# Kernel optimization log

Hardware: AMD Instinct MI355X
Metric: run time of the kernel (lower is better)

## Reference

```python
import jax, jax.numpy as jnp
from jax import lax
import numpy as np

N_LABELS = 48
START = 46
END = 47


def _viterbi_forward(emission_scores, transition, lengths):
    # scores[b, t, i, j]: score of transitioning from label i to label j at step t
    scores = emission_scores + transition  # [B, T, L, L]
    B, T, L, _ = scores.shape
    lengths = lengths.astype(jnp.int32)

    # ---- t == 0 ----
    mask0 = (lengths > 0)[:, None]  # [B, 1]
    first = scores[:, 0, START, :]  # [B, L]
    best0 = jnp.where(mask0, first, 0.0)
    upto0 = jnp.where(mask0, first, 0.0)
    bp0 = jnp.where(mask0, jnp.int32(START), jnp.int32(END))
    bp0 = jnp.broadcast_to(bp0, (B, L))

    # ---- t = 1 .. T-1 via scan (inherently sequential DP) ----
    def step(carry, inp):
        best, upto = carry  # each [B, L]
        s_t, t = inp  # s_t: [B, L, L]
        mask = (lengths > t)[:, None]  # [B, 1]
        cand = s_t + best[:, :, None]  # [B, from, to]
        new_best = jnp.max(cand, axis=1)  # [B, L]
        bp = jnp.argmax(cand, axis=1).astype(jnp.int32)  # [B, L]
        new_upto = jax.scipy.special.logsumexp(s_t + upto[:, :, None], axis=1)
        best = jnp.where(mask, new_best, best)
        upto = jnp.where(mask, new_upto, upto)
        bp = jnp.where(mask, bp, jnp.int32(END))
        return (best, upto), bp

    ts = jnp.arange(1, T, dtype=jnp.int32)
    scores_rest = jnp.swapaxes(scores[:, 1:], 0, 1)  # [T-1, B, L, L]
    (best, upto), bps = lax.scan(step, (best0, upto0), (scores_rest, ts))
    backpointers = jnp.concatenate([bp0[None], bps], axis=0)  # [T, B, L]

    # ---- backtracking (reverse scan over time) ----
    pointer0 = jnp.full((B,), END, dtype=jnp.int32)

    def back(ptr, bp_t):  # bp_t: [B, L]
        dec = jnp.take_along_axis(bp_t, ptr[:, None], axis=1)[:, 0]
        return dec, dec

    _, decoded = lax.scan(back, pointer0, backpointers, reverse=True)  # [T, B]
    decoded = decoded.T  # [B, T]
    # drop the initial start-label column, append end label
    decoded = jnp.concatenate(
        [decoded[:, 1:], jnp.full((B, 1), END, dtype=decoded.dtype)], axis=1
    )
    score_out = -(upto[:, END] - best[:, END])  # [B]
    return decoded, score_out


def setup_inputs() -> dict:
    key = jax.random.key(0)
    k1, k2, k3 = jax.random.split(key, 3)
    B, T, L = 32, 256, N_LABELS
    emission_scores = jax.random.normal(k1, (B, T, L, L), dtype=jnp.float32)
    transition = jax.random.normal(k2, (L, L), dtype=jnp.float32)
    lengths = jax.random.randint(k3, (B,), 128, T + 1, dtype=jnp.int64)
    lengths = lengths.at[0].set(T)  # ensure max(lengths) == T (padded length)
    return {"emission_scores": emission_scores, "transition": transition, "lengths": lengths}


def reference(emission_scores, transition, lengths):
    return _viterbi_forward(emission_scores, transition, lengths)
```

## Files before the change

### kernel.cpp

```cpp
#include <hip/hip_runtime.h>


#define TT 256
#define LL 48
#define LSTART 46
#define LEND 47
#define BB 32
#define NL 64

#define BARRIER() do { \
    asm volatile("s_waitcnt lgkmcnt(0)" ::: "memory"); \
    __builtin_amdgcn_s_barrier(); \
  } while (0)

#define LOADROW(BUF, ROW) do { \
    int r_ = (ROW) < (TT - 1) ? (ROW) : (TT - 1); \
    const float* q_ = base + (size_t)r_ * (LL*LL); \
    _Pragma("unroll") \
    for (int k = 0; k < 12; ++k) (BUF)[k] = q_[k*LL]; \
  } while (0)

#define AMAX(vx, ix, vy, iy) do { \
    if ((vy) > (vx)) { (vx) = (vy); (ix) = (iy); } } while (0)

#define RL(var, lane) __int_as_float(__builtin_amdgcn_readlane(__float_as_int(var), (lane)))

#define STEP_V(BUF, T_, PAR) do { \
    float cv[12]; int ci[12]; \
    _Pragma("unroll") \
    for (int k = 0; k < 12; ++k) { \
      cv[k] = (BUF)[k] + trg[k] + RL(vbest, 12*w + k); \
      ci[k] = 12*w + k; \
    } \
    AMAX(cv[0],ci[0],cv[1],ci[1]);  AMAX(cv[2],ci[2],cv[3],ci[3]); \
    AMAX(cv[4],ci[4],cv[5],ci[5]);  AMAX(cv[6],ci[6],cv[7],ci[7]); \
    AMAX(cv[8],ci[8],cv[9],ci[9]);  AMAX(cv[10],ci[10],cv[11],ci[11]); \
    AMAX(cv[0],ci[0],cv[2],ci[2]);  AMAX(cv[4],ci[4],cv[6],ci[6]); \
    AMAX(cv[8],ci[8],cv[10],ci[10]); \
    AMAX(cv[0],ci[0],cv[4],ci[4]); \
    AMAX(cv[0],ci[0],cv[8],ci[8]); \
    partV[PAR][w][j] = make_float2(cv[0], __int_as_float(ci[0])); \
    BARRIER(); \
    float2 m0 = partV[PAR][0][j], m1 = partV[PAR][1][j]; \
    float2 m2 = partV[PAR][2][j], m3 = partV[PAR][3][j]; \
    float bv = m0.x; int ba = __float_as_int(m0.y); \
    AMAX(bv, ba, m1.x, __float_as_int(m1.y)); \
    AMAX(bv, ba, m2.x, __float_as_int(m2.y)); \
    AMAX(bv, ba, m3.x, __float_as_int(m3.y)); \
    bool upd = act && ((T_) < len); \
    vbest = upd ? bv : vbest; \
    if (w == 0 && upd) bp[(T_)*LL + j] = (unsigned char)ba; \
  } while (0)

#define STEP_L(BUF, T_, PAR) do { \
    float e[12]; \
    _Pragma("unroll") \
    for (int k = 0; k < 12; ++k) { \
      float x = (BUF)[k] + trg[k] + RL(vupto, 12*w + k); \
      e[k] = exp2f((x - msh) * 1.44269504f); \
    } \
    float s01 = e[0]+e[1], s23 = e[2]+e[3], s45 = e[4]+e[5]; \
    float s67 = e[6]+e[7], s89 = e[8]+e[9], sab = e[10]+e[11]; \
    float ps = ((s01+s23)+(s45+s67)) + (s89+sab); \
    partS[PAR][w][j] = ps; \
    BARRIER(); \
    float sum = partS[PAR][0][j] + partS[PAR][1][j] \
              + partS[PAR][2][j] + partS[PAR][3][j]; \
    float nu = msh + log2f(sum) * 0.69314718056f; \
    bool upd = act && ((T_) < len); \
    vupto = upd ? nu : vupto; \
    msh = RL(vupto, 0); \
  } while (0)

__launch_bounds__(256, 1)
__global__ void viterbi_fwd(const float* __restrict__ em,
                            const float* __restrict__ tr,
                            const int* __restrict__ len_raw,
                            float* __restrict__ out,
                            float* __restrict__ ws)
{
  const int role = blockIdx.x >> 5;
  const int b    = blockIdx.x & 31;
  const int tid  = threadIdx.x;
  const int w    = tid >> 6;
  const int j    = tid & 63;
  const bool act = (j < LL);
  const int jl   = act ? j : (LL - 1);

  int len;
  {
    bool is64 = (len_raw[1] == 0) && (len_raw[3] == 0) && (len_raw[5] == 0);
    len = is64 ? len_raw[2*b] : len_raw[b];
    if (len > TT) len = TT;
    if (len < 1) len = 1;
  }

  __shared__ float2 partV[2][4][NL];
  __shared__ float  partS[2][4][NL];
  __shared__ unsigned char bp[TT*LL];
  __shared__ unsigned char cmp_[16*LL];
  __shared__ unsigned char entry_[16];
  __shared__ unsigned char raw[TT];

  float trg[12];
  #pragma unroll
  for (int k = 0; k < 12; ++k) trg[k] = tr[(12*w + k)*LL + jl];

  const float init = em[(size_t)b*TT*LL*LL + LSTART*LL + jl] + tr[LSTART*LL + jl];

  const float* base = em + (size_t)b*TT*LL*LL + (size_t)(12*w)*LL + jl;
  float b0[12], b1[12], b2[12], b3[12];

  if (role == 0) {
    for (int idx = tid; idx < LL; idx += 256) bp[idx] = (unsigned char)LSTART;
    for (int idx = len*LL + tid; idx < TT*LL; idx += 256) bp[idx] = (unsigned char)LEND;

    float vbest = act ? init : -INFINITY;
    LOADROW(b0, 1); LOADROW(b1, 2); LOADROW(b2, 3);
    int t = 1;
    #pragma unroll 1
    for (int it = 0; it < 63; ++it) {
      LOADROW(b3, t + 3); STEP_V(b0, t,     0);
      LOADROW(b0, t + 4); STEP_V(b1, t + 1, 1);
      LOADROW(b1, t + 5); STEP_V(b2, t + 2, 0);
      LOADROW(b2, t + 6); STEP_V(b3, t + 3, 1);
      t += 4;
    }
    STEP_V(b0, 253, 0); STEP_V(b1, 254, 1); STEP_V(b2, 255, 0);

    if (tid == LEND) ws[BB + b] = vbest;
    __syncthreads();

    for (int idx = tid; idx < 16*LL; idx += 256) {
      int c = idx / LL, l = idx - c*LL;
      int pc = l;
      #pragma unroll
      for (int k = 15; k >= 0; --k) pc = bp[(16*c + k)*LL + pc];
      cmp_[c*LL + l] = (unsigned char)pc;
    }
    __syncthreads();
    if (tid == 0) {
      int pc = LEND;
      for (int c = 15; c >= 0; --c) { entry_[c] = (unsigned char)pc; pc = cmp_[c*LL + pc]; }
    }
    __syncthreads();
    if (tid < 16) {
      int c = tid, pc = entry_[c];
      #pragma unroll
      for (int k = 15; k >= 0; --k) { int t2 = 16*c + k; pc = bp[t2*LL + pc]; raw[t2] = (unsigned char)pc; }
    }
    __syncthreads();
    out[(size_t)b*TT + tid] = (tid < TT - 1) ? (float)raw[tid + 1] : (float)LEND;
  } else {
    float vupto = act ? init : -INFINITY;
    float msh = RL(vupto, 0);
    LOADROW(b0, 1); LOADROW(b1, 2); LOADROW(b2, 3);
    int t = 1;
    #pragma unroll 1
    for (int it = 0; it < 63; ++it) {
      LOADROW(b3, t + 3); STEP_L(b0, t,     0);
      LOADROW(b0, t + 4); STEP_L(b1, t + 1, 1);
      LOADROW(b1, t + 5); STEP_L(b2, t + 2, 0);
      LOADROW(b2, t + 6); STEP_L(b3, t + 3, 1);
      t += 4;
    }
    STEP_L(b0, 253, 0); STEP_L(b1, 254, 1); STEP_L(b2, 255, 0);

    if (tid == LEND) ws[b] = vupto;
  }
}

__global__ void viterbi_score(const float* __restrict__ ws, float* __restrict__ out)
{
  int b = threadIdx.x;
  if (b < BB) out[(size_t)BB*TT + b] = ws[BB + b] - ws[b];
}

extern "C" void kernel_launch(void* const* d_in, const int* in_sizes, int n_in,
                              void* d_out, int out_size, void* d_ws, size_t ws_size,
                              hipStream_t stream) {
  const float* em  = (const float*)d_in[0];
  const float* tr  = (const float*)d_in[1];
  const int*   ln  = (const int*)d_in[2];
  float* out = (float*)d_out;
  float* ws  = (float*)d_ws;
  viterbi_fwd<<<dim3(64), dim3(256), 0, stream>>>(em, tr, ln, out, ws);
  viterbi_score<<<dim3(1), dim3(64), 0, stream>>>(ws, out);
}
```

Measured before the change: 144.3 us.

## Stream emission rows into an LDS ring via async global_load_lds prefetch

Replaces per-thread register prefetch of emission rows with asynchronous global-to-LDS loads into an 8-row shared ring buffer, issued in groups of four rows and waited on once per four steps. Each step reads the next row from LDS and precomputes emission+transition (scaled to log2 domain for the logsumexp path) ahead of the barrier. The Viterbi path also splits value and index partials, and only wave 0 resolves the argmax. The goal is to hide global memory latency behind the sequential DP, at the cost of much larger LDS usage and fragile hand-managed vmcnt waits.

```diff
diff --git a/kernel.cpp b/kernel.cpp
--- a/kernel.cpp
+++ b/kernel.cpp
@@ -1,37 +1,46 @@
 #include <hip/hip_runtime.h>
+#include <stdint.h>
 
 
 #define TT 256
 #define LL 48
+#define ROWF 2304
 #define LSTART 46
 #define LEND 47
 #define BB 32
 #define NL 64
-
-#define BARRIER() do { \
-    asm volatile("s_waitcnt lgkmcnt(0)" ::: "memory"); \
-    __builtin_amdgcn_s_barrier(); \
+#define LOG2E 1.44269504088896f
+#define LN2 0.693147180559945f
+
+#define GLL(GP, LP) __builtin_amdgcn_global_load_lds( \
+    (const __attribute__((address_space(1))) void*)(GP), \
+    (__attribute__((address_space(3))) void*)(LP), 16, 0, 0)
+
+#define FENCE() asm volatile("" ::: "memory")
+#define WAIT_PLAIN() asm volatile("s_waitcnt lgkmcnt(0)" ::: "memory")
+#define WAIT_VM0()   asm volatile("s_waitcnt vmcnt(0) lgkmcnt(0)" ::: "memory")
+
+#define AMAX(vx, ix, vy, iy) do { if ((vy) > (vx)) { (vx)=(vy); (ix)=(iy);} } while(0)
+#define RL(var, lane) __int_as_float(__builtin_amdgcn_readlane(__float_as_int(var), (lane)))
+
+#define ISSUE_GROUP(GR0, HB) do { \
+    const float* gs_ = em_lane + (size_t)(GR0)*ROWF; \
+    float* ls_ = ring + (HB); \
+    _Pragma("unroll") \
+    for (int ii = 0; ii < 9; ++ii) \
+      GLL(gs_ + (w*9+ii)*256, ls_ + (w*9+ii)*256); \
   } while (0)
 
-#define LOADROW(BUF, ROW) do { \
-    int r_ = (ROW) < (TT - 1) ? (ROW) : (TT - 1); \
-    const float* q_ = base + (size_t)r_ * (LL*LL); \
-    _Pragma("unroll") \
-    for (int k = 0; k < 12; ++k) (BUF)[k] = q_[k*LL]; \
-  } while (0)
-
-#define AMAX(vx, ix, vy, iy) do { \
-    if ((vy) > (vx)) { (vx) = (vy); (ix) = (iy); } } while (0)
-
-#define RL(var, lane) __int_as_float(__builtin_amdgcn_readlane(__float_as_int(var), (lane)))
-
-#define STEP_V(BUF, T_, PAR) do { \
+#define STEP_V(ETRC, ETRN, T_, WAITM) do { \
+    const int PAR_ = (T_) & 1; \
+    float en_[12]; \
+    { const float* lp_ = ring + (size_t)(((T_)+1)&7)*ROWF + jl; \
+      _Pragma("unroll") \
+      for (int k = 0; k < 12; ++k) en_[k] = lp_[(12*w+k)*LL]; } \
     float cv[12]; int ci[12]; \
     _Pragma("unroll") \
     for (int k = 0; k < 12; ++k) { \
-      cv[k] = (BUF)[k] + trg[k] + RL(vbest, 12*w + k); \
-      ci[k] = 12*w + k; \
-    } \
+      cv[k] = (ETRC)[k] + RL(vbest, lanebase+k); ci[k] = lanebase+k; } \
     AMAX(cv[0],ci[0],cv[1],ci[1]);  AMAX(cv[2],ci[2],cv[3],ci[3]); \
     AMAX(cv[4],ci[4],cv[5],ci[5]);  AMAX(cv[6],ci[6],cv[7],ci[7]); \
     AMAX(cv[8],ci[8],cv[9],ci[9]);  AMAX(cv[10],ci[10],cv[11],ci[11]); \
@@ -39,37 +48,53 @@
     AMAX(cv[8],ci[8],cv[10],ci[10]); \
     AMAX(cv[0],ci[0],cv[4],ci[4]); \
     AMAX(cv[0],ci[0],cv[8],ci[8]); \
-    partV[PAR][w][j] = make_float2(cv[0], __int_as_float(ci[0])); \
-    BARRIER(); \
-    float2 m0 = partV[PAR][0][j], m1 = partV[PAR][1][j]; \
-    float2 m2 = partV[PAR][2][j], m3 = partV[PAR][3][j]; \
-    float bv = m0.x; int ba = __float_as_int(m0.y); \
-    AMAX(bv, ba, m1.x, __float_as_int(m1.y)); \
-    AMAX(bv, ba, m2.x, __float_as_int(m2.y)); \
-    AMAX(bv, ba, m3.x, __float_as_int(m3.y)); \
-    bool upd = act && ((T_) < len); \
-    vbest = upd ? bv : vbest; \
-    if (w == 0 && upd) bp[(T_)*LL + j] = (unsigned char)ba; \
+    partVal[PAR_][w][j] = cv[0]; \
+    partIdx[PAR_][w][j] = ci[0]; \
+    _Pragma("unroll") \
+    for (int k = 0; k < 12; ++k) (ETRN)[k] = en_[k] + trg[k]; \
+    WAITM(); \
+    __builtin_amdgcn_s_barrier(); \
+    FENCE(); \
+    float v0_ = partVal[PAR_][0][j], v1_ = partVal[PAR_][1][j]; \
+    float v2_ = partVal[PAR_][2][j], v3_ = partVal[PAR_][3][j]; \
+    const bool upd_ = act && ((T_) < len); \
+    float bv_ = fmaxf(fmaxf(v0_, v1_), fmaxf(v2_, v3_)); \
+    vbest = upd_ ? bv_ : vbest; \
+    if (w == 0 && upd_) { \
+      float bx_ = v0_; int ba_ = partIdx[PAR_][0][j]; \
+      AMAX(bx_, ba_, v1_, partIdx[PAR_][1][j]); \
+      AMAX(bx_, ba_, v2_, partIdx[PAR_][2][j]); \
+      AMAX(bx_, ba_, v3_, partIdx[PAR_][3][j]); \
+      bp[(T_)*LL + j] = (unsigned char)ba_; \
+    } \
   } while (0)
 
-#define STEP_L(BUF, T_, PAR) do { \
-    float e[12]; \
+#define STEP_L(ETRC, ETRN, T_, WAITM) do { \
+    const int PAR_ = (T_) & 1; \
+    float en_[12]; \
+    { const float* lp_ = ring + (size_t)(((T_)+1)&7)*ROWF + jl; \
+      _Pragma("unroll") \
+      for (int k = 0; k < 12; ++k) en_[k] = lp_[(12*w+k)*LL]; } \
+    float ex[12]; \
     _Pragma("unroll") \
     for (int k = 0; k < 12; ++k) { \
-      float x = (BUF)[k] + trg[k] + RL(vupto, 12*w + k); \
-      e[k] = exp2f((x - msh) * 1.44269504f); \
+      float d_ = (ETRC)[k] - msh2; \
+      ex[k] = exp2f(d_ + RL(vupto2, lanebase+k)); \
     } \
-    float s01 = e[0]+e[1], s23 = e[2]+e[3], s45 = e[4]+e[5]; \
-    float s67 = e[6]+e[7], s89 = e[8]+e[9], sab = e[10]+e[11]; \
-    float ps = ((s01+s23)+(s45+s67)) + (s89+sab); \
-    partS[PAR][w][j] = ps; \
-    BARRIER(); \
-    float sum = partS[PAR][0][j] + partS[PAR][1][j] \
-              + partS[PAR][2][j] + partS[PAR][3][j]; \
-    float nu = msh + log2f(sum) * 0.69314718056f; \
-    bool upd = act && ((T_) < len); \
-    vupto = upd ? nu : vupto; \
-    msh = RL(vupto, 0); \
+    float s01=ex[0]+ex[1], s23=ex[2]+ex[3], s45=ex[4]+ex[5]; \
+    float s67=ex[6]+ex[7], s89=ex[8]+ex[9], sab=ex[10]+ex[11]; \
+    partVal[PAR_][w][j] = ((s01+s23)+(s45+s67))+(s89+sab); \
+    _Pragma("unroll") \
+    for (int k = 0; k < 12; ++k) (ETRN)[k] = (en_[k] + trg[k]) * LOG2E; \
+    WAITM(); \
+    __builtin_amdgcn_s_barrier(); \
+    FENCE(); \
+    float sum_ = (partVal[PAR_][0][j] + partVal[PAR_][1][j]) \
+               + (partVal[PAR_][2][j] + partVal[PAR_][3][j]); \
+    float nu_ = msh2 + __log2f(sum_); \
+    const bool upd_ = act && ((T_) < len); \
+    vupto2 = upd_ ? nu_ : vupto2; \
+    msh2 = RL(vupto2, 0); \
   } while (0)
 
 __launch_bounds__(256, 1)
@@ -86,6 +111,7 @@
   const int j    = tid & 63;
   const bool act = (j < LL);
   const int jl   = act ? j : (LL - 1);
+  const int lanebase = 12*w;
 
   int len;
   {
@@ -95,38 +121,51 @@
     if (len < 1) len = 1;
   }
 
-  __shared__ float2 partV[2][4][NL];
-  __shared__ float  partS[2][4][NL];
+  __shared__ float ring[8*ROWF];
+  __shared__ float partVal[2][4][NL];
+  __shared__ int   partIdx[2][4][NL];
   __shared__ unsigned char bp[TT*LL];
   __shared__ unsigned char cmp_[16*LL];
   __shared__ unsigned char entry_[16];
   __shared__ unsigned char raw[TT];
 
+  const float* em_lane = em + (size_t)b*TT*ROWF + 4*j;
+
   float trg[12];
   #pragma unroll
-  for (int k = 0; k < 12; ++k) trg[k] = tr[(12*w + k)*LL + jl];
-
-  const float init = em[(size_t)b*TT*LL*LL + LSTART*LL + jl] + tr[LSTART*LL + jl];
-
-  const float* base = em + (size_t)b*TT*LL*LL + (size_t)(12*w)*LL + jl;
-  float b0[12], b1[12], b2[12], b3[12];
+  for (int k = 0; k < 12; ++k) trg[k] = tr[(12*w+k)*LL + jl];
+
+  ISSUE_GROUP(0, 0);
+  ISSUE_GROUP(4, 4*ROWF);
+  asm volatile("s_waitcnt vmcnt(9)" ::: "memory");
+  __builtin_amdgcn_s_barrier();
+  FENCE();
+
+  const float init = ring[LSTART*LL + jl] + tr[LSTART*LL + jl];
 
   if (role == 0) {
     for (int idx = tid; idx < LL; idx += 256) bp[idx] = (unsigned char)LSTART;
     for (int idx = len*LL + tid; idx < TT*LL; idx += 256) bp[idx] = (unsigned char)LEND;
 
     float vbest = act ? init : -INFINITY;
-    LOADROW(b0, 1); LOADROW(b1, 2); LOADROW(b2, 3);
-    int t = 1;
+    float etrA[12], etrB[12];
+    { const float* lp_ = ring + ROWF + jl;
+      #pragma unroll
+      for (int k = 0; k < 12; ++k) etrA[k] = lp_[(12*w+k)*LL] + trg[k]; }
+
     #pragma unroll 1
     for (int it = 0; it < 63; ++it) {
-      LOADROW(b3, t + 3); STEP_V(b0, t,     0);
-      LOADROW(b0, t + 4); STEP_V(b1, t + 1, 1);
-      LOADROW(b1, t + 5); STEP_V(b2, t + 2, 0);
-      LOADROW(b2, t + 6); STEP_V(b3, t + 3, 1);
-      t += 4;
-    }
-    STEP_V(b0, 253, 0); STEP_V(b1, 254, 1); STEP_V(b2, 255, 0);
+      const int t0 = 4*it + 1;
+      STEP_V(etrA, etrB, t0,     WAIT_PLAIN);
+      STEP_V(etrB, etrA, t0 + 1, WAIT_VM0);
+      { int gr0 = 4*it + 8; if (gr0 > 252) gr0 = 252;
+        ISSUE_GROUP(gr0, (size_t)(it & 1)*4*ROWF); }
+      STEP_V(etrA, etrB, t0 + 2, WAIT_PLAIN);
+      STEP_V(etrB, etrA, t0 + 3, WAIT_PLAIN);
+    }
+    STEP_V(etrA, etrB, 253, WAIT_PLAIN);
+    STEP_V(etrB, etrA, 254, WAIT_VM0);
+    STEP_V(etrA, etrB, 255, WAIT_PLAIN);
 
     if (tid == LEND) ws[BB + b] = vbest;
     __syncthreads();
@@ -152,21 +191,28 @@
     __syncthreads();
     out[(size_t)b*TT + tid] = (tid < TT - 1) ? (float)raw[tid + 1] : (float)LEND;
   } else {
-    float vupto = act ? init : -INFINITY;
-    float msh = RL(vupto, 0);
-    LOADROW(b0, 1); LOADROW(b1, 2); LOADROW(b2, 3);
-    int t = 1;
+    float vupto2 = act ? init * LOG2E : -INFINITY;
+    float msh2 = RL(vupto2, 0);
+    float etrA[12], etrB[12];
+    { const float* lp_ = ring + ROWF + jl;
+      #pragma unroll
+      for (int k = 0; k < 12; ++k) etrA[k] = (lp_[(12*w+k)*LL] + trg[k]) * LOG2E; }
+
     #pragma unroll 1
     for (int it = 0; it < 63; ++it) {
-      LOADROW(b3, t + 3); STEP_L(b0, t,     0);
-      LOADROW(b0, t + 4); STEP_L(b1, t + 1, 1);
-      LOADROW(b1, t + 5); STEP_L(b2, t + 2, 0);
-      LOADROW(b2, t + 6); STEP_L(b3, t + 3, 1);
-      t += 4;
-    }
-    STEP_L(b0, 253, 0); STEP_L(b1, 254, 1); STEP_L(b2, 255, 0);
-
-    if (tid == LEND) ws[b] = vupto;
+      const int t0 = 4*it + 1;
+      STEP_L(etrA, etrB, t0,     WAIT_PLAIN);
+      STEP_L(etrB, etrA, t0 + 1, WAIT_VM0);
+      { int gr0 = 4*it + 8; if (gr0 > 252) gr0 = 252;
+        ISSUE_GROUP(gr0, (size_t)(it & 1)*4*ROWF); }
+      STEP_L(etrA, etrB, t0 + 2, WAIT_PLAIN);
+      STEP_L(etrB, etrA, t0 + 3, WAIT_PLAIN);
+    }
+    STEP_L(etrA, etrB, 253, WAIT_PLAIN);
+    STEP_L(etrB, etrA, 254, WAIT_VM0);
+    STEP_L(etrA, etrB, 255, WAIT_PLAIN);
+
+    if (tid == LEND) ws[b] = vupto2 * LN2;
   }
 }
 
```

Result: slower. 155.5 us (+7.8%).

## Stage emission rows via global_load_lds ring and switch logsumexp to linear-domain scaling

Applied to the files above, without the earlier changes.

Emission rows are now prefetched asynchronously into a six-slot LDS ring with global_load_lds, replacing per-thread register prefetch. The loop is software-pipelined so the reduction of the previous step overlaps with computing the next step's partials, with one barrier per step. The logsumexp path now works in the probability domain: it exponentiates emissions plus transitions independently of the recurrence, combines them with FMAs against a scaled state vector, and renormalises by extracting the exponent, which removes the per-step log and the dependence of exp on the carried state. The risks are precision and underflow in the scaled linear domain, plus the extra LDS footprint and the subtle ring-slot and vmcnt bookkeeping.

```diff
diff --git a/kernel.cpp b/kernel.cpp
--- a/kernel.cpp
+++ b/kernel.cpp
@@ -3,35 +3,43 @@
 
 #define TT 256
 #define LL 48
+#define ROWF 2304
 #define LSTART 46
 #define LEND 47
 #define BB 32
-#define NL 64
+#define LOG2E 1.44269504088896f
+#define LN2 0.693147180559945f
+
+#define GLL16(GP, LP) __builtin_amdgcn_global_load_lds( \
+    (const __attribute__((address_space(1))) void*)(GP), \
+    (__attribute__((address_space(3))) void*)(LP), 16, 0, 0)
+#define GLL4(GP, LP) __builtin_amdgcn_global_load_lds( \
+    (const __attribute__((address_space(1))) void*)(GP), \
+    (__attribute__((address_space(3))) void*)(LP), 4, 0, 0)
+
+#define RL(var, lane) __int_as_float(__builtin_amdgcn_readlane(__float_as_int(var), (lane)))
 
 #define BARRIER() do { \
     asm volatile("s_waitcnt lgkmcnt(0)" ::: "memory"); \
     __builtin_amdgcn_s_barrier(); \
   } while (0)
-
-#define LOADROW(BUF, ROW) do { \
-    int r_ = (ROW) < (TT - 1) ? (ROW) : (TT - 1); \
-    const float* q_ = base + (size_t)r_ * (LL*LL); \
-    _Pragma("unroll") \
-    for (int k = 0; k < 12; ++k) (BUF)[k] = q_[k*LL]; \
-  } while (0)
-
-#define AMAX(vx, ix, vy, iy) do { \
-    if ((vy) > (vx)) { (vx) = (vy); (ix) = (iy); } } while (0)
-
-#define RL(var, lane) __int_as_float(__builtin_amdgcn_readlane(__float_as_int(var), (lane)))
-
-#define STEP_V(BUF, T_, PAR) do { \
+#define WAITVM(N) asm volatile("s_waitcnt vmcnt(" #N ")" ::: "memory")
+
+#define AMAX(vx, ix, vy, iy) do { if ((vy) > (vx)) { (vx)=(vy); (ix)=(iy);} } while(0)
+
+#define STAGE(ROW, SLOT) do { \
+    const float* gs_ = emB + (size_t)(ROW)*ROWF + wslice; \
+    float* ls_ = ring + (SLOT)*ROWF + wslice; \
+    GLL16(gs_ + 4*j, ls_); \
+    GLL16(gs_ + 256 + 4*j, ls_ + 256); \
+    GLL4 (gs_ + 512 + j, ls_ + 512); \
+  } while (0)
+
+#define PARTIALS_V(ETR, PW) do { \
     float cv[12]; int ci[12]; \
     _Pragma("unroll") \
     for (int k = 0; k < 12; ++k) { \
-      cv[k] = (BUF)[k] + trg[k] + RL(vbest, 12*w + k); \
-      ci[k] = 12*w + k; \
-    } \
+      cv[k] = (ETR)[k] + RL(vbest, 12*w + k); ci[k] = 12*w + k; } \
     AMAX(cv[0],ci[0],cv[1],ci[1]);  AMAX(cv[2],ci[2],cv[3],ci[3]); \
     AMAX(cv[4],ci[4],cv[5],ci[5]);  AMAX(cv[6],ci[6],cv[7],ci[7]); \
     AMAX(cv[8],ci[8],cv[9],ci[9]);  AMAX(cv[10],ci[10],cv[11],ci[11]); \
@@ -39,38 +47,78 @@
     AMAX(cv[8],ci[8],cv[10],ci[10]); \
     AMAX(cv[0],ci[0],cv[4],ci[4]); \
     AMAX(cv[0],ci[0],cv[8],ci[8]); \
-    partV[PAR][w][j] = make_float2(cv[0], __int_as_float(ci[0])); \
+    partV[PW][w][j] = make_float2(cv[0], __int_as_float(ci[0])); \
+  } while (0)
+
+#define ITER_V(T_, RAWP, RAWN) do { \
+    const int pr_ = ((T_)-1) & 1; \
+    float2 m0_ = partV[pr_][0][j], m1_ = partV[pr_][1][j]; \
+    float2 m2_ = partV[pr_][2][j], m3_ = partV[pr_][3][j]; \
+    float etr_[12]; \
+    _Pragma("unroll") \
+    for (int k = 0; k < 12; ++k) etr_[k] = (RAWP)[k] + trg[k]; \
+    { int row_ = (T_) + 5; if (row_ > 255) row_ = 255; \
+      STAGE(row_, sw); sw = (sw == 5) ? 0 : sw + 1; } \
+    WAITVM(12); \
+    { const float* rp_ = ring + sr*ROWF + jl; \
+      _Pragma("unroll") \
+      for (int k = 0; k < 12; ++k) (RAWN)[k] = rp_[(12*w+k)*LL]; \
+      sr = (sr == 5) ? 0 : sr + 1; } \
+    float bv_ = m0_.x; int ba_ = __float_as_int(m0_.y); \
+    AMAX(bv_, ba_, m1_.x, __float_as_int(m1_.y)); \
+    AMAX(bv_, ba_, m2_.x, __float_as_int(m2_.y)); \
+    AMAX(bv_, ba_, m3_.x, __float_as_int(m3_.y)); \
+    { const bool upd_ = act && (((T_)-1) < len); \
+      vbest = upd_ ? bv_ : vbest; \
+      if (w == 0 && upd_) bp[((T_)-1)*LL + j] = (unsigned char)ba_; } \
+    PARTIALS_V(etr_, (T_) & 1); \
     BARRIER(); \
-    float2 m0 = partV[PAR][0][j], m1 = partV[PAR][1][j]; \
-    float2 m2 = partV[PAR][2][j], m3 = partV[PAR][3][j]; \
-    float bv = m0.x; int ba = __float_as_int(m0.y); \
-    AMAX(bv, ba, m1.x, __float_as_int(m1.y)); \
-    AMAX(bv, ba, m2.x, __float_as_int(m2.y)); \
-    AMAX(bv, ba, m3.x, __float_as_int(m3.y)); \
-    bool upd = act && ((T_) < len); \
-    vbest = upd ? bv : vbest; \
-    if (w == 0 && upd) bp[(T_)*LL + j] = (unsigned char)ba; \
-  } while (0)
-
-#define STEP_L(BUF, T_, PAR) do { \
-    float e[12]; \
-    _Pragma("unroll") \
-    for (int k = 0; k < 12; ++k) { \
-      float x = (BUF)[k] + trg[k] + RL(vupto, 12*w + k); \
-      e[k] = exp2f((x - msh) * 1.44269504f); \
+  } while (0)
+
+#define PARTIALS_L(EE, PW) do { \
+    float a0 = 0.f, a1 = 0.f, a2 = 0.f, a3 = 0.f; \
+    _Pragma("unroll") \
+    for (int k = 0; k < 12; k += 4) { \
+      a0 = fmaf((EE)[k+0], RL(P, 12*w + k + 0), a0); \
+      a1 = fmaf((EE)[k+1], RL(P, 12*w + k + 1), a1); \
+      a2 = fmaf((EE)[k+2], RL(P, 12*w + k + 2), a2); \
+      a3 = fmaf((EE)[k+3], RL(P, 12*w + k + 3), a3); \
     } \
-    float s01 = e[0]+e[1], s23 = e[2]+e[3], s45 = e[4]+e[5]; \
-    float s67 = e[6]+e[7], s89 = e[8]+e[9], sab = e[10]+e[11]; \
-    float ps = ((s01+s23)+(s45+s67)) + (s89+sab); \
-    partS[PAR][w][j] = ps; \
+    partS[PW][w][j] = (a0 + a1) + (a2 + a3); \
+  } while (0)
+
+#define ITER_L(T_, RAWP, RAWN) do { \
+    const int pr_ = ((T_)-1) & 1; \
+    float s0_ = partS[pr_][0][j], s1_ = partS[pr_][1][j]; \
+    float s2_ = partS[pr_][2][j], s3_ = partS[pr_][3][j]; \
+    float ee_[12]; \
+    _Pragma("unroll") \
+    for (int k = 0; k < 12; ++k) \
+      ee_[k] = exp2f(fmaf((RAWP)[k], LOG2E, trg2[k])); \
+    { int row_ = (T_) + 5; if (row_ > 255) row_ = 255; \
+      STAGE(row_, sw); sw = (sw == 5) ? 0 : sw + 1; } \
+    WAITVM(12); \
+    { const float* rp_ = ring + sr*ROWF + jl; \
+      _Pragma("unroll") \
+      for (int k = 0; k < 12; ++k) (RAWN)[k] = rp_[(12*w+k)*LL]; \
+      sr = (sr == 5) ? 0 : sr + 1; } \
+    float Pn_ = (s0_ + s1_) + (s2_ + s3_); \
+    { int rb_ = __builtin_amdgcn_readlane(__float_as_int(Pn_), 0); \
+      int e_ = ((rb_ >> 23) & 255) - 127; \
+      const bool upd_ = (((T_)-1) < len); \
+      P    = upd_ ? __builtin_ldexpf(Pn_, -e_) : P; \
+      macc = upd_ ? macc + (float)e_ : macc; } \
+    PARTIALS_L(ee_, (T_) & 1); \
     BARRIER(); \
-    float sum = partS[PAR][0][j] + partS[PAR][1][j] \
-              + partS[PAR][2][j] + partS[PAR][3][j]; \
-    float nu = msh + log2f(sum) * 0.69314718056f; \
-    bool upd = act && ((T_) < len); \
-    vupto = upd ? nu : vupto; \
-    msh = RL(vupto, 0); \
-  } while (0)
+  } while (0)
+
+__device__ __forceinline__ int load_len(const int* len_raw, int b) {
+  bool is64 = (len_raw[1] == 0) && (len_raw[3] == 0) && (len_raw[5] == 0);
+  int len = is64 ? len_raw[2*b] : len_raw[b];
+  if (len > TT) len = TT;
+  if (len < 1) len = 1;
+  return len;
+}
 
 __launch_bounds__(256, 1)
 __global__ void viterbi_fwd(const float* __restrict__ em,
@@ -86,48 +134,65 @@
   const int j    = tid & 63;
   const bool act = (j < LL);
   const int jl   = act ? j : (LL - 1);
-
-  int len;
-  {
-    bool is64 = (len_raw[1] == 0) && (len_raw[3] == 0) && (len_raw[5] == 0);
-    len = is64 ? len_raw[2*b] : len_raw[b];
-    if (len > TT) len = TT;
-    if (len < 1) len = 1;
-  }
-
-  __shared__ float2 partV[2][4][NL];
-  __shared__ float  partS[2][4][NL];
+  const int wslice = w * 576;
+  const int len  = load_len(len_raw, b);
+
+  __shared__ float ring[6*ROWF];
+  __shared__ float2 partV[2][4][64];
+  __shared__ float  partS[2][4][64];
   __shared__ unsigned char bp[TT*LL];
   __shared__ unsigned char cmp_[16*LL];
   __shared__ unsigned char entry_[16];
   __shared__ unsigned char raw[TT];
 
-  float trg[12];
-  #pragma unroll
-  for (int k = 0; k < 12; ++k) trg[k] = tr[(12*w + k)*LL + jl];
-
-  const float init = em[(size_t)b*TT*LL*LL + LSTART*LL + jl] + tr[LSTART*LL + jl];
-
-  const float* base = em + (size_t)b*TT*LL*LL + (size_t)(12*w)*LL + jl;
-  float b0[12], b1[12], b2[12], b3[12];
+  const float* emB = em + (size_t)b*TT*ROWF;
 
   if (role == 0) {
     for (int idx = tid; idx < LL; idx += 256) bp[idx] = (unsigned char)LSTART;
     for (int idx = len*LL + tid; idx < TT*LL; idx += 256) bp[idx] = (unsigned char)LEND;
-
+    __syncthreads();
+
+    float trg[12];
+    #pragma unroll
+    for (int k = 0; k < 12; ++k) trg[k] = tr[(12*w + k)*LL + jl];
+    const float init = emB[LSTART*LL + jl] + tr[LSTART*LL + jl];
     float vbest = act ? init : -INFINITY;
-    LOADROW(b0, 1); LOADROW(b1, 2); LOADROW(b2, 3);
-    int t = 1;
+
+    STAGE(1,1); STAGE(2,2); STAGE(3,3); STAGE(4,4); STAGE(5,5); STAGE(6,0);
+    WAITVM(15);
+    float rawA[12], rawB[12];
+    {
+      const float* rp = ring + 1*ROWF + jl;
+      float e1[12];
+      #pragma unroll
+      for (int k = 0; k < 12; ++k) e1[k] = rp[(12*w+k)*LL] + trg[k];
+      PARTIALS_V(e1, 1);
+    }
+    WAITVM(12);
+    {
+      const float* rp = ring + 2*ROWF + jl;
+      #pragma unroll
+      for (int k = 0; k < 12; ++k) rawA[k] = rp[(12*w+k)*LL];
+    }
+    BARRIER();
+
+    int sr = 3, sw = 1;
     #pragma unroll 1
-    for (int it = 0; it < 63; ++it) {
-      LOADROW(b3, t + 3); STEP_V(b0, t,     0);
-      LOADROW(b0, t + 4); STEP_V(b1, t + 1, 1);
-      LOADROW(b1, t + 5); STEP_V(b2, t + 2, 0);
-      LOADROW(b2, t + 6); STEP_V(b3, t + 3, 1);
-      t += 4;
-    }
-    STEP_V(b0, 253, 0); STEP_V(b1, 254, 1); STEP_V(b2, 255, 0);
-
+    for (int t = 2; t <= 254; t += 2) {
+      ITER_V(t,     rawA, rawB);
+      ITER_V(t + 1, rawB, rawA);
+    }
+    {
+      float2 m0 = partV[1][0][j], m1 = partV[1][1][j];
+      float2 m2 = partV[1][2][j], m3 = partV[1][3][j];
+      float bv = m0.x; int ba = __float_as_int(m0.y);
+      AMAX(bv, ba, m1.x, __float_as_int(m1.y));
+      AMAX(bv, ba, m2.x, __float_as_int(m2.y));
+      AMAX(bv, ba, m3.x, __float_as_int(m3.y));
+      const bool upd = act && (255 < len);
+      vbest = upd ? bv : vbest;
+      if (w == 0 && upd) bp[255*LL + j] = (unsigned char)ba;
+    }
     if (tid == LEND) ws[BB + b] = vbest;
     __syncthreads();
 
@@ -151,22 +216,50 @@
     }
     __syncthreads();
     out[(size_t)b*TT + tid] = (tid < TT - 1) ? (float)raw[tid + 1] : (float)LEND;
+
   } else {
-    float vupto = act ? init : -INFINITY;
-    float msh = RL(vupto, 0);
-    LOADROW(b0, 1); LOADROW(b1, 2); LOADROW(b2, 3);
-    int t = 1;
+    float trg2[12];
+    #pragma unroll
+    for (int k = 0; k < 12; ++k) trg2[k] = tr[(12*w + k)*LL + jl] * LOG2E;
+    const float init = emB[LSTART*LL + jl] + tr[LSTART*LL + jl];
+    const float m2 = RL(init, 0) * LOG2E;
+    float P = act ? exp2f(init * LOG2E - m2) : 0.f;
+    float macc = m2;
+
+    STAGE(1,1); STAGE(2,2); STAGE(3,3); STAGE(4,4); STAGE(5,5); STAGE(6,0);
+    WAITVM(15);
+    float rawA[12], rawB[12];
+    {
+      const float* rp = ring + 1*ROWF + jl;
+      float e1[12];
+      #pragma unroll
+      for (int k = 0; k < 12; ++k) e1[k] = exp2f(fmaf(rp[(12*w+k)*LL], LOG2E, trg2[k]));
+      PARTIALS_L(e1, 1);
+    }
+    WAITVM(12);
+    {
+      const float* rp = ring + 2*ROWF + jl;
+      #pragma unroll
+      for (int k = 0; k < 12; ++k) rawA[k] = rp[(12*w+k)*LL];
+    }
+    BARRIER();
+
+    int sr = 3, sw = 1;
     #pragma unroll 1
-    for (int it = 0; it < 63; ++it) {
-      LOADROW(b3, t + 3); STEP_L(b0, t,     0);
-      LOADROW(b0, t + 4); STEP_L(b1, t + 1, 1);
-      LOADROW(b1, t + 5); STEP_L(b2, t + 2, 0);
-      LOADROW(b2, t + 6); STEP_L(b3, t + 3, 1);
-      t += 4;
-    }
-    STEP_L(b0, 253, 0); STEP_L(b1, 254, 1); STEP_L(b2, 255, 0);
-
-    if (tid == LEND) ws[b] = vupto;
+    for (int t = 2; t <= 254; t += 2) {
+      ITER_L(t,     rawA, rawB);
+      ITER_L(t + 1, rawB, rawA);
+    }
+    {
+      float Pn = (partS[1][0][j] + partS[1][1][j])
+               + (partS[1][2][j] + partS[1][3][j]);
+      int rb = __builtin_amdgcn_readlane(__float_as_int(Pn), 0);
+      int e  = ((rb >> 23) & 255) - 127;
+      const bool upd = (255 < len);
+      P    = upd ? __builtin_ldexpf(Pn, -e) : P;
+      macc = upd ? macc + (float)e : macc;
+    }
+    if (tid == LEND) ws[b] = (macc + __log2f(P)) * LN2;
   }
 }
 
```

After: 184.8 us. 28.0% more time.

## Halve barriers by doing odd steps wave-redundantly; logsumexp in linear scaled domain

Applied to the files above, without the earlier changes.

Each block now alternates two kinds of timestep. Even steps keep the 4-wave split reduction through shared memory. Odd steps are computed redundantly by every wave over all 48 source labels in registers, which removes half of the barriers on the sequential critical path. The logsumexp path now carries a probability vector P plus an exponent accumulator, renormalised by powers of two. This turns each step into exp plus FMA dot products, with no max-shift and no log per step. The cost is four times the odd-step loads and arithmetic, much higher register pressure from the 48-wide buffers, and some risk from underflow or overflow in the scaled linear domain.

```diff
diff --git a/kernel.cpp b/kernel.cpp
--- a/kernel.cpp
+++ b/kernel.cpp
@@ -3,35 +3,70 @@
 
 #define TT 256
 #define LL 48
+#define ROWF 2304
 #define LSTART 46
 #define LEND 47
 #define BB 32
-#define NL 64
+#define LOG2E 1.44269504088896f
+#define LN2 0.693147180559945f
+
+#define RL(var, lane) __int_as_float(__builtin_amdgcn_readlane(__float_as_int(var), (lane)))
 
 #define BARRIER() do { \
     asm volatile("s_waitcnt lgkmcnt(0)" ::: "memory"); \
     __builtin_amdgcn_s_barrier(); \
   } while (0)
 
-#define LOADROW(BUF, ROW) do { \
-    int r_ = (ROW) < (TT - 1) ? (ROW) : (TT - 1); \
-    const float* q_ = base + (size_t)r_ * (LL*LL); \
-    _Pragma("unroll") \
-    for (int k = 0; k < 12; ++k) (BUF)[k] = q_[k*LL]; \
-  } while (0)
-
-#define AMAX(vx, ix, vy, iy) do { \
-    if ((vy) > (vx)) { (vx) = (vy); (ix) = (iy); } } while (0)
-
-#define RL(var, lane) __int_as_float(__builtin_amdgcn_readlane(__float_as_int(var), (lane)))
-
-#define STEP_V(BUF, T_, PAR) do { \
+#define PIN12(B) asm volatile("" : \
+    "+v"((B)[0]), "+v"((B)[1]), "+v"((B)[2]),  "+v"((B)[3]), \
+    "+v"((B)[4]), "+v"((B)[5]), "+v"((B)[6]),  "+v"((B)[7]), \
+    "+v"((B)[8]), "+v"((B)[9]), "+v"((B)[10]), "+v"((B)[11]))
+#define PIN48(B) do { PIN12(B); PIN12((B)+12); PIN12((B)+24); PIN12((B)+36); } while (0)
+
+#define LOADROW12(B, ROW) do { \
+    const float* q_ = emB + (size_t)(ROW)*ROWF + (size_t)(12*w)*LL + jl; \
+    _Pragma("unroll") \
+    for (int k = 0; k < 12; ++k) (B)[k] = q_[k*LL]; \
+  } while (0)
+#define LOADROW48(B, ROW) do { \
+    const float* q_ = emB + (size_t)(ROW)*ROWF + jl; \
+    _Pragma("unroll") \
+    for (int i = 0; i < 48; ++i) (B)[i] = q_[i*LL]; \
+  } while (0)
+
+#define AMAX(vx, ix, vy, iy) do { if ((vy) > (vx)) { (vx)=(vy); (ix)=(iy);} } while(0)
+
+#define ODD_V(B48C, T_) do { \
+    _Pragma("unroll") \
+    for (int i = 0; i < 48; ++i) (B48C)[i] += RL(vbest, i); \
+    float mt_[16]; \
+    _Pragma("unroll") \
+    for (int i = 0; i < 16; ++i) \
+      mt_[i] = fmaxf(fmaxf((B48C)[i], (B48C)[i+16]), (B48C)[i+32]); \
+    _Pragma("unroll") \
+    for (int i = 0; i < 8; ++i) mt_[i] = fmaxf(mt_[i], mt_[i+8]); \
+    _Pragma("unroll") \
+    for (int i = 0; i < 4; ++i) mt_[i] = fmaxf(mt_[i], mt_[i+4]); \
+    float bv2_ = fmaxf(fmaxf(mt_[0], mt_[1]), fmaxf(mt_[2], mt_[3])); \
+    const bool u2_ = act && ((T_) < len); \
+    if (w == 0 && u2_) {   \
+      int id_ = 0; \
+      _Pragma("unroll") \
+      for (int i = 47; i >= 0; --i) if ((B48C)[i] == bv2_) id_ = i; \
+      bp[(T_)*LL + j] = (unsigned char)id_; \
+    } \
+    vbest = u2_ ? bv2_ : vbest; \
+  } while (0)
+
+#define ROUND_V(R_, B12C, B48C, B12N, B48N) do { \
+    PIN12(B12C); \
+    float etr_[12]; \
+    _Pragma("unroll") \
+    for (int k = 0; k < 12; ++k) etr_[k] = (B12C)[k] + trg12[k]; \
     float cv[12]; int ci[12]; \
     _Pragma("unroll") \
     for (int k = 0; k < 12; ++k) { \
-      cv[k] = (BUF)[k] + trg[k] + RL(vbest, 12*w + k); \
-      ci[k] = 12*w + k; \
-    } \
+      cv[k] = etr_[k] + RL(vbest, 12*w + k); ci[k] = 12*w + k; } \
     AMAX(cv[0],ci[0],cv[1],ci[1]);  AMAX(cv[2],ci[2],cv[3],ci[3]); \
     AMAX(cv[4],ci[4],cv[5],ci[5]);  AMAX(cv[6],ci[6],cv[7],ci[7]); \
     AMAX(cv[8],ci[8],cv[9],ci[9]);  AMAX(cv[10],ci[10],cv[11],ci[11]); \
@@ -39,38 +74,82 @@
     AMAX(cv[8],ci[8],cv[10],ci[10]); \
     AMAX(cv[0],ci[0],cv[4],ci[4]); \
     AMAX(cv[0],ci[0],cv[8],ci[8]); \
-    partV[PAR][w][j] = make_float2(cv[0], __int_as_float(ci[0])); \
+    partV[w][j] = make_float2(cv[0], __int_as_float(ci[0])); \
+    { int rn_ = 2*(R_) + 2; if (rn_ > 255) rn_ = 255; LOADROW12(B12N, rn_); } \
+    { int rn_ = 2*(R_) + 3; if (rn_ > 255) rn_ = 255; LOADROW48(B48N, rn_); } \
+    PIN48(B48C); \
+    _Pragma("unroll") \
+    for (int i = 0; i < 48; ++i) (B48C)[i] += trg48[i]; \
     BARRIER(); \
-    float2 m0 = partV[PAR][0][j], m1 = partV[PAR][1][j]; \
-    float2 m2 = partV[PAR][2][j], m3 = partV[PAR][3][j]; \
-    float bv = m0.x; int ba = __float_as_int(m0.y); \
-    AMAX(bv, ba, m1.x, __float_as_int(m1.y)); \
-    AMAX(bv, ba, m2.x, __float_as_int(m2.y)); \
-    AMAX(bv, ba, m3.x, __float_as_int(m3.y)); \
-    bool upd = act && ((T_) < len); \
-    vbest = upd ? bv : vbest; \
-    if (w == 0 && upd) bp[(T_)*LL + j] = (unsigned char)ba; \
-  } while (0)
-
-#define STEP_L(BUF, T_, PAR) do { \
-    float e[12]; \
-    _Pragma("unroll") \
-    for (int k = 0; k < 12; ++k) { \
-      float x = (BUF)[k] + trg[k] + RL(vupto, 12*w + k); \
-      e[k] = exp2f((x - msh) * 1.44269504f); \
-    } \
-    float s01 = e[0]+e[1], s23 = e[2]+e[3], s45 = e[4]+e[5]; \
-    float s67 = e[6]+e[7], s89 = e[8]+e[9], sab = e[10]+e[11]; \
-    float ps = ((s01+s23)+(s45+s67)) + (s89+sab); \
-    partS[PAR][w][j] = ps; \
+    { \
+      float2 m0_ = partV[0][j], m1_ = partV[1][j]; \
+      float2 m2_ = partV[2][j], m3_ = partV[3][j]; \
+      float bv_ = m0_.x; int ba_ = __float_as_int(m0_.y); \
+      AMAX(bv_, ba_, m1_.x, __float_as_int(m1_.y)); \
+      AMAX(bv_, ba_, m2_.x, __float_as_int(m2_.y)); \
+      AMAX(bv_, ba_, m3_.x, __float_as_int(m3_.y)); \
+      const bool u_ = act && (2*(R_) < len); \
+      vbest = u_ ? bv_ : vbest; \
+      if (w == 0 && u_) bp[2*(R_)*LL + j] = (unsigned char)ba_; \
+    } \
+    ODD_V(B48C, 2*(R_) + 1); \
+  } while (0)
+
+#define ODD_L(B48C, T_) do { \
+    float a0_ = 0.f, a1_ = 0.f, a2_ = 0.f, a3_ = 0.f; \
+    _Pragma("unroll") \
+    for (int i = 0; i < 48; i += 4) { \
+      a0_ = fmaf((B48C)[i+0], RL(P, i+0), a0_); \
+      a1_ = fmaf((B48C)[i+1], RL(P, i+1), a1_); \
+      a2_ = fmaf((B48C)[i+2], RL(P, i+2), a2_); \
+      a3_ = fmaf((B48C)[i+3], RL(P, i+3), a3_); \
+    } \
+    float Pn_ = (a0_ + a1_) + (a2_ + a3_); \
+    int rb_ = __builtin_amdgcn_readlane(__float_as_int(Pn_), 0); \
+    int e_  = ((rb_ >> 23) & 255) - 127; \
+    const bool u2_ = ((T_) < len); \
+    P    = u2_ ? __builtin_ldexpf(Pn_, -e_) : P; \
+    macc = u2_ ? macc + (float)e_ : macc; \
+  } while (0)
+
+#define ROUND_L(R_, B12C, B48C, B12N, B48N) do { \
+    PIN12(B12C); \
+    float ee_[12]; \
+    _Pragma("unroll") \
+    for (int k = 0; k < 12; ++k) ee_[k] = exp2f(fmaf((B12C)[k], LOG2E, trg12[k])); \
+    { float a0_=0.f, a1_=0.f, a2_=0.f, a3_=0.f; \
+      _Pragma("unroll") \
+      for (int k = 0; k < 12; k += 4) { \
+        a0_ = fmaf(ee_[k+0], RL(P, 12*w + k + 0), a0_); \
+        a1_ = fmaf(ee_[k+1], RL(P, 12*w + k + 1), a1_); \
+        a2_ = fmaf(ee_[k+2], RL(P, 12*w + k + 2), a2_); \
+        a3_ = fmaf(ee_[k+3], RL(P, 12*w + k + 3), a3_); \
+      } \
+      partS[w][j] = (a0_ + a1_) + (a2_ + a3_); } \
+    { int rn_ = 2*(R_) + 2; if (rn_ > 255) rn_ = 255; LOADROW12(B12N, rn_); } \
+    { int rn_ = 2*(R_) + 3; if (rn_ > 255) rn_ = 255; LOADROW48(B48N, rn_); } \
+    PIN48(B48C); \
+    _Pragma("unroll") \
+    for (int i = 0; i < 48; ++i) (B48C)[i] = exp2f(fmaf((B48C)[i], LOG2E, trg48[i])); \
     BARRIER(); \
-    float sum = partS[PAR][0][j] + partS[PAR][1][j] \
-              + partS[PAR][2][j] + partS[PAR][3][j]; \
-    float nu = msh + log2f(sum) * 0.69314718056f; \
-    bool upd = act && ((T_) < len); \
-    vupto = upd ? nu : vupto; \
-    msh = RL(vupto, 0); \
-  } while (0)
+    { \
+      float Pn_ = (partS[0][j] + partS[1][j]) + (partS[2][j] + partS[3][j]); \
+      int rb_ = __builtin_amdgcn_readlane(__float_as_int(Pn_), 0); \
+      int e_  = ((rb_ >> 23) & 255) - 127; \
+      const bool u_ = (2*(R_) < len); \
+      P    = u_ ? __builtin_ldexpf(Pn_, -e_) : P; \
+      macc = u_ ? macc + (float)e_ : macc; \
+    } \
+    ODD_L(B48C, 2*(R_) + 1); \
+  } while (0)
+
+__device__ __forceinline__ int load_len(const int* len_raw, int b) {
+  bool is64 = (len_raw[1] == 0) && (len_raw[3] == 0) && (len_raw[5] == 0);
+  int len = is64 ? len_raw[2*b] : len_raw[b];
+  if (len > TT) len = TT;
+  if (len < 1) len = 1;
+  return len;
+}
 
 __launch_bounds__(256, 1)
 __global__ void viterbi_fwd(const float* __restrict__ em,
@@ -86,47 +165,47 @@
   const int j    = tid & 63;
   const bool act = (j < LL);
   const int jl   = act ? j : (LL - 1);
-
-  int len;
-  {
-    bool is64 = (len_raw[1] == 0) && (len_raw[3] == 0) && (len_raw[5] == 0);
-    len = is64 ? len_raw[2*b] : len_raw[b];
-    if (len > TT) len = TT;
-    if (len < 1) len = 1;
-  }
-
-  __shared__ float2 partV[2][4][NL];
-  __shared__ float  partS[2][4][NL];
+  const int len  = load_len(len_raw, b);
+
+  __shared__ float2 partV[4][64];
+  __shared__ float  partS[4][64];
   __shared__ unsigned char bp[TT*LL];
   __shared__ unsigned char cmp_[16*LL];
   __shared__ unsigned char entry_[16];
   __shared__ unsigned char raw[TT];
 
-  float trg[12];
+  const float* emB = em + (size_t)b*TT*ROWF;
+
+  float trg48[48];
   #pragma unroll
-  for (int k = 0; k < 12; ++k) trg[k] = tr[(12*w + k)*LL + jl];
-
-  const float init = em[(size_t)b*TT*LL*LL + LSTART*LL + jl] + tr[LSTART*LL + jl];
-
-  const float* base = em + (size_t)b*TT*LL*LL + (size_t)(12*w)*LL + jl;
-  float b0[12], b1[12], b2[12], b3[12];
+  for (int i = 0; i < 48; ++i) trg48[i] = tr[i*LL + jl];
 
   if (role == 0) {
     for (int idx = tid; idx < LL; idx += 256) bp[idx] = (unsigned char)LSTART;
     for (int idx = len*LL + tid; idx < TT*LL; idx += 256) bp[idx] = (unsigned char)LEND;
-
+    __syncthreads();
+
+    float trg12[12];
+    #pragma unroll
+    for (int k = 0; k < 12; ++k) trg12[k] = trg48[12*w + k];
+    const float init = emB[LSTART*LL + jl] + trg48[LSTART];
     float vbest = act ? init : -INFINITY;
-    LOADROW(b0, 1); LOADROW(b1, 2); LOADROW(b2, 3);
-    int t = 1;
+
+    float B12O[12], B12E[12], B48O[48], B48E[48];
+    LOADROW48(B48E, 1);
+    LOADROW12(B12O, 2);
+    LOADROW48(B48O, 3);
+    PIN48(B48E);
+    #pragma unroll
+    for (int i = 0; i < 48; ++i) B48E[i] += trg48[i];
+    ODD_V(B48E, 1);
+
     #pragma unroll 1
-    for (int it = 0; it < 63; ++it) {
-      LOADROW(b3, t + 3); STEP_V(b0, t,     0);
-      LOADROW(b0, t + 4); STEP_V(b1, t + 1, 1);
-      LOADROW(b1, t + 5); STEP_V(b2, t + 2, 0);
-      LOADROW(b2, t + 6); STEP_V(b3, t + 3, 1);
-      t += 4;
-    }
-    STEP_V(b0, 253, 0); STEP_V(b1, 254, 1); STEP_V(b2, 255, 0);
+    for (int m = 0; m < 63; ++m) {
+      ROUND_V(2*m + 1, B12O, B48O, B12E, B48E);
+      ROUND_V(2*m + 2, B12E, B48E, B12O, B48O);
+    }
+    ROUND_V(127, B12O, B48O, B12E, B48E);
 
     if (tid == LEND) ws[BB + b] = vbest;
     __syncthreads();
@@ -151,22 +230,36 @@
     }
     __syncthreads();
     out[(size_t)b*TT + tid] = (tid < TT - 1) ? (float)raw[tid + 1] : (float)LEND;
+
   } else {
-    float vupto = act ? init : -INFINITY;
-    float msh = RL(vupto, 0);
-    LOADROW(b0, 1); LOADROW(b1, 2); LOADROW(b2, 3);
-    int t = 1;
+    float trg12[12];
+    #pragma unroll
+    for (int k = 0; k < 12; ++k) trg12[k] = trg48[12*w + k] * LOG2E;
+    #pragma unroll
+    for (int i = 0; i < 48; ++i) trg48[i] *= LOG2E;
+
+    const float init = emB[LSTART*LL + jl] + tr[LSTART*LL + jl];
+    const float m2 = RL(init, 0) * LOG2E;
+    float P = act ? exp2f(init * LOG2E - m2) : 0.f;
+    float macc = m2;
+
+    float B12O[12], B12E[12], B48O[48], B48E[48];
+    LOADROW48(B48E, 1);
+    LOADROW12(B12O, 2);
+    LOADROW48(B48O, 3);
+    PIN48(B48E);
+    #pragma unroll
+    for (int i = 0; i < 48; ++i) B48E[i] = exp2f(fmaf(B48E[i], LOG2E, trg48[i]));
+    ODD_L(B48E, 1);
+
     #pragma unroll 1
-    for (int it = 0; it < 63; ++it) {
-      LOADROW(b3, t + 3); STEP_L(b0, t,     0);
-      LOADROW(b0, t + 4); STEP_L(b1, t + 1, 1);
-      LOADROW(b1, t + 5); STEP_L(b2, t + 2, 0);
-      LOADROW(b2, t + 6); STEP_L(b3, t + 3, 1);
-      t += 4;
-    }
-    STEP_L(b0, 253, 0); STEP_L(b1, 254, 1); STEP_L(b2, 255, 0);
-
-    if (tid == LEND) ws[b] = vupto;
+    for (int m = 0; m < 63; ++m) {
+      ROUND_L(2*m + 1, B12O, B48O, B12E, B48E);
+      ROUND_L(2*m + 2, B12E, B48E, B12O, B48O);
+    }
+    ROUND_L(127, B12O, B48O, B12E, B48E);
+
+    if (tid == LEND) ws[b] = (macc + __log2f(P)) * LN2;
   }
 }
 
```

Result: slower. 254.3 us (+76.2%).
